# Performance work log

Hardware: AMD Instinct MI355X
Metric: run time of the kernel (lower is better)

Reference implementation:

```python
import jax, jax.numpy as jnp
import numpy as np

B, H, W = 64, 84, 84
IN_F, HID, NCLS = 128, 256, 50
C2 = IN_F * 2  # 256
EPS = 1e-5
K_NEIGH = 4


def _ring_edges(batch):
    rows = np.repeat(np.arange(batch), K_NEIGH)
    offs = np.tile(np.arange(1, K_NEIGH + 1), batch)
    cols = (rows + offs) % batch
    return jnp.asarray(np.stack([rows, cols]), dtype=jnp.int32)


def setup_inputs() -> dict:
    key = jax.random.key(0)
    ks = jax.random.split(key, 40)
    i = iter(range(40))
    def n(shape, s=0.05):
        return jax.random.normal(ks[next(i)], shape, jnp.float32) * s
    def u(shape):
        return jax.random.uniform(ks[next(i)], shape, jnp.float32, 0.5, 1.5)
    d = {}
    d['x'] = jax.random.normal(ks[next(i)], (B, 3, H, W), jnp.float32)
    # conv1 + bn1
    d['conv1_w'] = n((IN_F, 3, 3, 3)); d['conv1_b'] = n((IN_F,))
    d['bn1_g'] = 1.0 + n((IN_F,)); d['bn1_b'] = n((IN_F,))
    d['bn1_m'] = n((IN_F,)); d['bn1_v'] = u((IN_F,))
    # conv2 + bn2
    d['conv2_w'] = n((C2, IN_F, 3, 3)); d['conv2_b'] = n((C2,))
    d['bn2_g'] = 1.0 + n((C2,)); d['bn2_b'] = n((C2,))
    d['bn2_m'] = n((C2,)); d['bn2_v'] = u((C2,))
    # conv3 + bn3
    d['conv3_w'] = n((C2, C2, 3, 3)); d['conv3_b'] = n((C2,))
    d['bn3_g'] = 1.0 + n((C2,)); d['bn3_b'] = n((C2,))
    d['bn3_m'] = n((C2,)); d['bn3_v'] = u((C2,))
    # gcn1: Linear(256,256), attn Linear(512,1)
    d['gcn1_lw'] = n((HID, C2)); d['gcn1_lb'] = n((HID,))
    d['gcn1_aw'] = n((1, 2 * C2)); d['gcn1_ab'] = n((1,))
    # gcn2: Linear(256,256), attn Linear(512,1)
    d['gcn2_lw'] = n((HID, HID)); d['gcn2_lb'] = n((HID,))
    d['gcn2_aw'] = n((1, 2 * HID)); d['gcn2_ab'] = n((1,))
    # fc
    d['fc_w'] = n((NCLS, HID)); d['fc_b'] = n((NCLS,))
    d['edge_index'] = _ring_edges(B)  # [2, 4*B] deterministic ring graph
    return d


def _conv_bn_relu(x, w, b, g, be, m, v):
    y = jax.lax.conv_general_dilated(
        x, w, window_strides=(1, 1), padding='SAME',
        dimension_numbers=('NCHW', 'OIHW', 'NCHW')) + b[None, :, None, None]
    scale = (g / jnp.sqrt(v + EPS))[None, :, None, None]
    y = (y - m[None, :, None, None]) * scale + be[None, :, None, None]
    return jax.nn.relu(y)


def _gcn_conv(h, row, col, lw, lb, aw, ab):
    # h: [N, F]; edge gather -> attn MLP -> global softmax -> scatter-add
    ef = jnp.concatenate([h[row], h[col]], axis=1)          # [E, 2F]
    ew = jax.nn.leaky_relu(ef @ aw.T + ab, 0.01)            # [E, 1]
    ew = jax.nn.softmax(ew, axis=0)                          # softmax over all edges
    agg = jnp.zeros_like(h).at[row].add(h[col] * ew)        # [N, F]
    return agg @ lw.T + lb + h                               # linear + residual


def reference(x, conv1_w, conv1_b, bn1_g, bn1_b, bn1_m, bn1_v,
              conv2_w, conv2_b, bn2_g, bn2_b, bn2_m, bn2_v,
              conv3_w, conv3_b, bn3_g, bn3_b, bn3_m, bn3_v,
              gcn1_lw, gcn1_lb, gcn1_aw, gcn1_ab,
              gcn2_lw, gcn2_lb, gcn2_aw, gcn2_ab,
              fc_w, fc_b, edge_index):
    h = _conv_bn_relu(x, conv1_w, conv1_b, bn1_g, bn1_b, bn1_m, bn1_v)
    h = _conv_bn_relu(h, conv2_w, conv2_b, bn2_g, bn2_b, bn2_m, bn2_v)
    h = _conv_bn_relu(h, conv3_w, conv3_b, bn3_g, bn3_b, bn3_m, bn3_v)
    h = h.mean(axis=(2, 3))                                  # adaptive avg pool 1x1 + flatten -> [B, 256]
    row, col = edge_index[0], edge_index[1]
    h = jax.nn.relu(_gcn_conv(h, row, col, gcn1_lw, gcn1_lb, gcn1_aw, gcn1_ab))
    h = jax.nn.relu(_gcn_conv(h, row, col, gcn2_lw, gcn2_lb, gcn2_aw, gcn2_ab))
    return h @ fc_w.T + fc_b                                 # [B, 50]
```

## Files before the change

kernel.cpp:

```cpp
#include <hip/hip_runtime.h>
#include <hip/hip_bf16.h>

typedef __attribute__((ext_vector_type(8))) short bf16x8;
typedef __attribute__((ext_vector_type(4))) float f32x4;

#define DEV __device__ __forceinline__

static constexpr int Bn   = 64;
static constexpr int Hs   = 84;
static constexpr int HP   = 86;
static constexpr int C1c  = 128;
static constexpr int C2c  = 256;
static constexpr int NPOS = Hs * Hs;
static constexpr float EPSf = 1e-5f;

DEV __hip_bfloat16 f2b(float v) { return __float2bfloat16(v); }

DEV void gload16(const void* g, void* l) {
    __builtin_amdgcn_global_load_lds(
        (const __attribute__((address_space(1))) void*)g,
        (__attribute__((address_space(3))) void*)l, 16, 0, 0);
}

__global__ __launch_bounds__(128) void conv1_k(
    const float* __restrict__ x,
    const float* __restrict__ w,  const float* __restrict__ cb,
    const float* __restrict__ g,  const float* __restrict__ be,
    const float* __restrict__ mm, const float* __restrict__ vv,
    __hip_bfloat16* __restrict__ h1)
{
    __shared__ float xin[3][3][HP];
    int bi = blockIdx.x;
    int b = bi / Hs, y = bi % Hs;
    int t = threadIdx.x;

    for (int idx = t; idx < 3 * 3 * HP; idx += 128) {
        int ci = idx / (3 * HP);
        int r  = idx % (3 * HP);
        int dy = r / HP;
        int xx = r % HP;
        int iy = y + dy - 1;
        int ix = xx - 1;
        float v = 0.f;
        if (iy >= 0 && iy < Hs && ix >= 0 && ix < Hs)
            v = x[((size_t)(b * 3 + ci) * Hs + iy) * Hs + ix];
        xin[ci][dy][xx] = v;
    }
    int co = t;
    float wr[3][3][3];
    for (int ci = 0; ci < 3; ci++)
        for (int dy = 0; dy < 3; dy++)
            for (int dx = 0; dx < 3; dx++)
                wr[ci][dy][dx] = w[((co * 3 + ci) * 3 + dy) * 3 + dx];
    float scale = g[co] / sqrtf(vv[co] + EPSf);
    float bias  = (cb[co] - mm[co]) * scale + be[co];
    __syncthreads();

    for (int xp = 0; xp < Hs; xp++) {
        float acc = 0.f;
        #pragma unroll
        for (int ci = 0; ci < 3; ci++)
            #pragma unroll
            for (int dy = 0; dy < 3; dy++)
                #pragma unroll
                for (int dx = 0; dx < 3; dx++)
                    acc += xin[ci][dy][xp + dx] * wr[ci][dy][dx];
        float o = acc * scale + bias;
        o = o > 0.f ? o : 0.f;
        h1[((size_t)(b * HP + y + 1) * HP + (xp + 1)) * C1c + co] = f2b(o);
    }
}

template <int C>
__global__ void halo_zero(__hip_bfloat16* __restrict__ h)
{
    int i = blockIdx.x;
    int b = i / 340, p = i % 340;
    int y, xx;
    if (p < 86)       { y = 0;  xx = p; }
    else if (p < 172) { y = 85; xx = p - 86; }
    else if (p < 256) { xx = 0; y = p - 172 + 1; }
    else              { xx = 85; y = p - 256 + 1; }
    h[((size_t)(b * HP + y) * HP + xx) * C + threadIdx.x] = f2b(0.f);
}

template <int CIN>
__global__ void prep_w(const float* __restrict__ w, __hip_bfloat16* __restrict__ wm)
{
    int e  = blockIdx.x * 256 + threadIdx.x;
    int k  = e >> 8;
    int co = e & 255;
    int tap = k / CIN;
    int ci  = k % CIN;
    int ty = tap / 3, tx = tap % 3;
    wm[(size_t)(k >> 5) * 8192 + co * 32 + (k & 31)] =
        f2b(w[((size_t)(co * CIN + ci) * 3 + ty) * 3 + tx]);
}

__global__ void prep_sb(const float* __restrict__ cb, const float* __restrict__ g,
                        const float* __restrict__ be, const float* __restrict__ mm,
                        const float* __restrict__ vv, float* __restrict__ sb)
{
    int co = threadIdx.x;
    float s = g[co] / sqrtf(vv[co] + EPSf);
    sb[co] = s;
    sb[256 + co] = (cb[co] - mm[co]) * s + be[co];
}

__global__ void zero_f32(float* __restrict__ p)
{
    p[blockIdx.x * 256 + threadIdx.x] = 0.f;
}

template <int CIN, bool POOL>
__global__ __launch_bounds__(512, 2) void conv_igemm(
    const __hip_bfloat16* __restrict__ in, const __hip_bfloat16* __restrict__ wgt,
    const float* __restrict__ sb, __hip_bfloat16* __restrict__ out, float* __restrict__ pool)
{
    constexpr int KB = CIN / 32;
    constexpr int NK = 9 * KB / 2;
    constexpr unsigned BUF = 49152u;
    __shared__ __align__(16) char lds[3 * 49152];
    __shared__ float pl[512];

    int t = threadIdx.x;
    int l = t & 63, w = t >> 6;
    int lidx = l & 15, lg = l >> 4;
    int wm = w >> 2, wn = w & 3;

    int nwg  = (int)gridDim.x;
    int orig = (int)blockIdx.x;
    int xcd = orig & 7, idx = orig >> 3;
    int q = nwg >> 3, r = nwg & 7;
    int bx = (xcd < r ? xcd * (q + 1) : r * (q + 1) + (xcd - r) * q) + idx;
    int m0 = bx * 128;

    int seg  = (t & 3) ^ ((t >> 3) & 3);
    int srow = t >> 2;
    const __hip_bfloat16* pA;
    {
        int gm = m0 + srow;
        int b0 = gm / NPOS; int r0 = gm - b0 * NPOS;
        int y0 = r0 / Hs;   int x0 = r0 - y0 * Hs;
        pA = in + ((size_t)(b0 * HP + y0) * HP + x0) * CIN + seg * 8;
    }
    const __hip_bfloat16* pB = wgt + (size_t)srow * 32 + seg * 8;

    int swz = (lidx >> 1) & 3;
    unsigned aRd[4][2], bRd[4][2];
    #pragma unroll
    for (int mf = 0; mf < 4; mf++)
        #pragma unroll
        for (int kh = 0; kh < 2; kh++)
            aRd[mf][kh] = (unsigned)(kh * 8192 + (wm * 64 + mf * 16 + lidx) * 64 + ((lg ^ swz) * 16));
    #pragma unroll
    for (int nf = 0; nf < 4; nf++)
        #pragma unroll
        for (int kh = 0; kh < 2; kh++)
            bRd[nf][kh] = (unsigned)(16384 + kh * 16384 + (wn * 64 + nf * 16 + lidx) * 64 + ((lg ^ swz) * 16));

    f32x4 acc[4][4];
    #pragma unroll
    for (int i = 0; i < 4; i++)
        #pragma unroll
        for (int j = 0; j < 4; j++)
            acc[i][j] = (f32x4){0.f, 0.f, 0.f, 0.f};
    if (POOL) pl[t] = 0.f;

    auto AOFF = [&](int s) -> size_t {
        int kb = s / 9, tap = s - kb * 9;
        int ty = tap / 3, tx = tap - ty * 3;
        return (size_t)(ty * HP + tx) * CIN + kb * 32;
    };
    auto BOFF = [&](int s) -> size_t {
        int kb = s / 9, tap = s - kb * 9;
        return (size_t)(tap * KB + kb) * 8192;
    };
    auto ISSUE_P0 = [&](int kt2, unsigned nb) {
        int s0 = 2 * kt2, s1 = s0 + 1;
        gload16(pA + AOFF(s0), lds + nb +          w * 1024);
        gload16(pA + AOFF(s1), lds + nb +  8192 + w * 1024);
        gload16(pB + BOFF(s0), lds + nb + 16384 + w * 1024);
    };
    auto ISSUE_P1 = [&](int kt2, unsigned nb) {
        int s0 = 2 * kt2, s1 = s0 + 1;
        gload16(pB + BOFF(s0) + 4096, lds + nb + 24576 + w * 1024);
        gload16(pB + BOFF(s1),        lds + nb + 32768 + w * 1024);
        gload16(pB + BOFF(s1) + 4096, lds + nb + 40960 + w * 1024);
    };

    ISSUE_P0(0, 0u); ISSUE_P1(0, 0u);
    ISSUE_P0(1, BUF); ISSUE_P1(1, BUF);

    for (int kt = 0; kt < NK; ++kt) {
        unsigned cb = (unsigned)(kt % 3) * BUF;
        unsigned nb = (unsigned)((kt + 2) % 3) * BUF;
        bool more = (kt + 2) < NK;

        if (kt + 1 < NK) asm volatile("s_waitcnt vmcnt(6)" ::: "memory");
        else             asm volatile("s_waitcnt vmcnt(0)" ::: "memory");
        __builtin_amdgcn_s_barrier();

        bf16x8 av[4][2], bv0[2][2];
        #pragma unroll
        for (int mf = 0; mf < 4; mf++)
            #pragma unroll
            for (int kh = 0; kh < 2; kh++)
                av[mf][kh] = *(const bf16x8*)(lds + cb + aRd[mf][kh]);
        #pragma unroll
        for (int nf = 0; nf < 2; nf++)
            #pragma unroll
            for (int kh = 0; kh < 2; kh++)
                bv0[nf][kh] = *(const bf16x8*)(lds + cb + bRd[nf][kh]);
        if (more) ISSUE_P0(kt + 2, nb);
        __builtin_amdgcn_s_barrier();
        asm volatile("s_waitcnt lgkmcnt(0)" ::: "memory");
        __builtin_amdgcn_sched_barrier(0);
        __builtin_amdgcn_s_setprio(1);
        #pragma unroll
        for (int kh = 0; kh < 2; kh++)
            #pragma unroll
            for (int mf = 0; mf < 4; mf++)
                #pragma unroll
                for (int nf = 0; nf < 2; nf++)
                    acc[mf][nf] = __builtin_amdgcn_mfma_f32_16x16x32_bf16(
                        av[mf][kh], bv0[nf][kh], acc[mf][nf], 0, 0, 0);
        __builtin_amdgcn_s_setprio(0);

        __builtin_amdgcn_s_barrier();
        bf16x8 bv1[2][2];
        #pragma unroll
        for (int nf = 0; nf < 2; nf++)
            #pragma unroll
            for (int kh = 0; kh < 2; kh++)
                bv1[nf][kh] = *(const bf16x8*)(lds + cb + bRd[2 + nf][kh]);
        if (more) ISSUE_P1(kt + 2, nb);
        __builtin_amdgcn_s_barrier();
        asm volatile("s_waitcnt lgkmcnt(0)" ::: "memory");
        __builtin_amdgcn_sched_barrier(0);
        __builtin_amdgcn_s_setprio(1);
        #pragma unroll
        for (int kh = 0; kh < 2; kh++)
            #pragma unroll
            for (int mf = 0; mf < 4; mf++)
                #pragma unroll
                for (int nf = 0; nf < 2; nf++)
                    acc[mf][2 + nf] = __builtin_amdgcn_mfma_f32_16x16x32_bf16(
                        av[mf][kh], bv1[nf][kh], acc[mf][2 + nf], 0, 0, 0);
        __builtin_amdgcn_s_setprio(0);
    }

    float sc[4], bi2[4];
    #pragma unroll
    for (int nf = 0; nf < 4; nf++) {
        int cn = wn * 64 + nf * 16 + lidx;
        sc[nf]  = sb[cn];
        bi2[nf] = sb[256 + cn];
    }

    if (!POOL) {
        #pragma unroll
        for (int mf = 0; mf < 4; mf++) {
            #pragma unroll
            for (int r2 = 0; r2 < 4; r2++) {
                int row = wm * 64 + mf * 16 + lg * 4 + r2;
                int gm2 = m0 + row;
                int b2  = gm2 / NPOS;
                int rm2 = gm2 - b2 * NPOS;
                int y2  = rm2 / Hs;
                int x2  = rm2 - y2 * Hs;
                size_t ob = ((size_t)(b2 * HP + y2 + 1) * HP + (x2 + 1)) * 256;
                #pragma unroll
                for (int nf = 0; nf < 4; nf++) {
                    float v = acc[mf][nf][r2] * sc[nf] + bi2[nf];
                    v = v > 0.f ? v : 0.f;
                    out[ob + wn * 64 + nf * 16 + lidx] = f2b(v);
                }
            }
        }
    } else {
        int bs_lo   = m0 / NPOS;
        int row_lim = (bs_lo + 1) * NPOS - m0;
        __builtin_amdgcn_s_barrier();
        #pragma unroll
        for (int nf = 0; nf < 4; nf++) {
            float s0 = 0.f, s1 = 0.f;
            #pragma unroll
            for (int mf = 0; mf < 4; mf++)
                #pragma unroll
                for (int r2 = 0; r2 < 4; r2++) {
                    int row = wm * 64 + mf * 16 + lg * 4 + r2;
                    float v = acc[mf][nf][r2] * sc[nf] + bi2[nf];
                    v = v > 0.f ? v : 0.f;
                    if (row < row_lim) s0 += v; else s1 += v;
                }
            int cl = wn * 64 + nf * 16 + lidx;
            atomicAdd(&pl[cl], s0);
            if (row_lim < 128) atomicAdd(&pl[256 + cl], s1);
        }
        __syncthreads();
        if (t < 256)
            atomicAdd(&pool[bs_lo * 256 + t], pl[t]);
        else if (row_lim < 128)
            atomicAdd(&pool[(bs_lo + 1) * 256 + (t - 256)], pl[t]);
    }
}

__global__ void pool_div(const float* __restrict__ pool, float* __restrict__ h0)
{
    int i = blockIdx.x * 256 + threadIdx.x;
    h0[i] = pool[i] * (1.0f / (float)NPOS);
}

__global__ __launch_bounds__(256) void gcn_attn(
    const float* __restrict__ h, const float* __restrict__ aw,
    const float* __restrict__ ab, const int* __restrict__ ei,
    float* __restrict__ ew)
{
    __shared__ float p[64], q[64], red[256];
    int t = threadIdx.x;
    if (t < 64) {
        float pp = 0.f, qq = 0.f;
        for (int c = 0; c < 256; c++) {
            float hv = h[t * 256 + c];
            pp += hv * aw[c];
            qq += hv * aw[256 + c];
        }
        p[t] = pp; q[t] = qq;
    }
    __syncthreads();
    int r = ei[t], c = ei[256 + t];
    float s = p[r] + q[c] + ab[0];
    s = s >= 0.f ? s : 0.01f * s;
    red[t] = s;
    __syncthreads();
    for (int st = 128; st > 0; st >>= 1) {
        if (t < st) red[t] = fmaxf(red[t], red[t + st]);
        __syncthreads();
    }
    float mx = red[0];
    __syncthreads();
    float e = expf(s - mx);
    red[t] = e;
    __syncthreads();
    for (int st = 128; st > 0; st >>= 1) {
        if (t < st) red[t] += red[t + st];
        __syncthreads();
    }
    ew[t] = e / red[0];
}

__global__ __launch_bounds__(256) void gcn_agg(
    const float* __restrict__ h, const float* __restrict__ ew, const int* __restrict__ ei,
    const float* __restrict__ lw, const float* __restrict__ lb,
    float* __restrict__ ho)
{
    __shared__ float agg[256];
    __shared__ float ewl[256];
    __shared__ int rl[256], cl[256];
    int n = blockIdx.x;
    int t = threadIdx.x;
    ewl[t] = ew[t];
    rl[t] = ei[t];
    cl[t] = ei[256 + t];
    __syncthreads();
    float a = 0.f;
    for (int e = 0; e < 256; e++)
        if (rl[e] == n) a += ewl[e] * h[cl[e] * 256 + t];
    agg[t] = a;
    __syncthreads();
    float o = 0.f;
    for (int c2 = 0; c2 < 256; c2++)
        o += agg[c2] * lw[t * 256 + c2];
    o += lb[t] + h[n * 256 + t];
    o = o > 0.f ? o : 0.f;
    ho[n * 256 + t] = o;
}

__global__ void fc_k(const float* __restrict__ h, const float* __restrict__ fw,
                     const float* __restrict__ fb, float* __restrict__ out)
{
    int n = blockIdx.x;
    int t = threadIdx.x;
    if (t < 50) {
        float o = 0.f;
        for (int c = 0; c < 256; c++)
            o += h[n * 256 + c] * fw[t * 256 + c];
        o += fb[t];
        out[n * 50 + t] = o;
    }
}

extern "C" void kernel_launch(void* const* d_in, const int* in_sizes, int n_in,
                              void* d_out, int out_size, void* d_ws, size_t ws_size,
                              hipStream_t stream)
{
    (void)in_sizes; (void)n_in; (void)out_size;

    const float* X    = (const float*)d_in[0];
    const float* c1w  = (const float*)d_in[1];
    const float* c1b  = (const float*)d_in[2];
    const float* b1g  = (const float*)d_in[3];
    const float* b1b  = (const float*)d_in[4];
    const float* b1m  = (const float*)d_in[5];
    const float* b1v  = (const float*)d_in[6];
    const float* c2w  = (const float*)d_in[7];
    const float* c2b  = (const float*)d_in[8];
    const float* b2g  = (const float*)d_in[9];
    const float* b2b  = (const float*)d_in[10];
    const float* b2m  = (const float*)d_in[11];
    const float* b2v  = (const float*)d_in[12];
    const float* c3w  = (const float*)d_in[13];
    const float* c3b  = (const float*)d_in[14];
    const float* b3g  = (const float*)d_in[15];
    const float* b3b  = (const float*)d_in[16];
    const float* b3m  = (const float*)d_in[17];
    const float* b3v  = (const float*)d_in[18];
    const float* g1lw = (const float*)d_in[19];
    const float* g1lb = (const float*)d_in[20];
    const float* g1aw = (const float*)d_in[21];
    const float* g1ab = (const float*)d_in[22];
    const float* g2lw = (const float*)d_in[23];
    const float* g2lb = (const float*)d_in[24];
    const float* g2aw = (const float*)d_in[25];
    const float* g2ab = (const float*)d_in[26];
    const float* fcw  = (const float*)d_in[27];
    const float* fcb  = (const float*)d_in[28];
    const int*   EI   = (const int*)d_in[29];

    size_t fixedB = 3000000;
    int chb = 8;
    if (ws_size >= (size_t)64 * 5680128 + fixedB)      chb = 64;
    else if (ws_size >= (size_t)32 * 5680128 + fixedB) chb = 32;
    else if (ws_size >= (size_t)16 * 5680128 + fixedB) chb = 16;
    int nchunks = Bn / chb;
    int mch = chb * NPOS;

    char* p = (char*)d_ws;
    auto carve = [&](size_t bytes) {
        char* r = p;
        p += (bytes + 255) & ~(size_t)255;
        return r;
    };
    __hip_bfloat16* h1c = (__hip_bfloat16*)carve((size_t)chb * HP * HP * C1c * 2);
    __hip_bfloat16* h2c = (__hip_bfloat16*)carve((size_t)chb * HP * HP * C2c * 2);
    __hip_bfloat16* wm2 = (__hip_bfloat16*)carve((size_t)9 * C1c * 256 * 2);
    __hip_bfloat16* wm3 = (__hip_bfloat16*)carve((size_t)9 * C2c * 256 * 2);
    float* sb2  = (float*)carve(512 * 4);
    float* sb3  = (float*)carve(512 * 4);
    float* pool = (float*)carve(64 * 256 * 4);
    float* h0   = (float*)carve(64 * 256 * 4);
    float* hg1  = (float*)carve(64 * 256 * 4);
    float* hg2  = (float*)carve(64 * 256 * 4);
    float* ew1  = (float*)carve(256 * 4);
    float* ew2  = (float*)carve(256 * 4);

    halo_zero<C1c><<<dim3(chb * 340), dim3(C1c), 0, stream>>>(h1c);
    halo_zero<C2c><<<dim3(chb * 340), dim3(C2c), 0, stream>>>(h2c);
    prep_w<C1c><<<dim3(9 * C1c), dim3(256), 0, stream>>>(c2w, wm2);
    prep_w<C2c><<<dim3(9 * C2c), dim3(256), 0, stream>>>(c3w, wm3);
    prep_sb<<<dim3(1), dim3(256), 0, stream>>>(c2b, b2g, b2b, b2m, b2v, sb2);
    prep_sb<<<dim3(1), dim3(256), 0, stream>>>(c3b, b3g, b3b, b3m, b3v, sb3);
    zero_f32<<<dim3(64), dim3(256), 0, stream>>>(pool);

    for (int ch = 0; ch < nchunks; ch++) {
        const float* xch = X + (size_t)ch * chb * 3 * NPOS;
        conv1_k<<<dim3(chb * Hs), dim3(C1c), 0, stream>>>(
            xch, c1w, c1b, b1g, b1b, b1m, b1v, h1c);
        conv_igemm<C1c, false><<<dim3(mch / 128), dim3(512), 0, stream>>>(
            h1c, wm2, sb2, h2c, nullptr);
        conv_igemm<C2c, true ><<<dim3(mch / 128), dim3(512), 0, stream>>>(
            h2c, wm3, sb3, nullptr, pool + (size_t)ch * chb * 256);
    }
    pool_div<<<dim3(64), dim3(256), 0, stream>>>(pool, h0);

    gcn_attn<<<dim3(1), dim3(256), 0, stream>>>(h0, g1aw, g1ab, EI, ew1);
    gcn_agg<<<dim3(64), dim3(256), 0, stream>>>(h0, ew1, EI, g1lw, g1lb, hg1);
    gcn_attn<<<dim3(1), dim3(256), 0, stream>>>(hg1, g2aw, g2ab, EI, ew2);
    gcn_agg<<<dim3(64), dim3(256), 0, stream>>>(hg1, ew2, EI, g2lw, g2lb, hg2);
    fc_k<<<dim3(64), dim3(64), 0, stream>>>(hg2, fcw, fcb, (float*)d_out);
}
```

Measured before the change: 1.014 ms.

## Enlarge conv implicit-GEMM M tile to 256 with double-buffered LDS pipeline

Doubles the per-block output tile from 128 to 256 rows so each wave computes 8x4 MFMA fragments, reusing each loaded B fragment across twice as many A rows. The LDS pipeline changes from triple-buffered 48KB stages to double-buffered 64KB stages, and loads are issued per k-half with a one-stage prefetch. Grid size halves and the pooling epilogue limits are updated. The larger accumulator array raises register pressure against the (512,2) launch bounds, the 128KB of LDS may cut occupancy, and the shallower prefetch could expose memory latency. The minimum chunk size also rises from 8 to 16 batches.

```diff
diff --git a/kernel.cpp b/kernel.cpp
--- a/kernel.cpp
+++ b/kernel.cpp
@@ -119,8 +119,8 @@
 {
     constexpr int KB = CIN / 32;
     constexpr int NK = 9 * KB / 2;
-    constexpr unsigned BUF = 49152u;
-    __shared__ __align__(16) char lds[3 * 49152];
+    constexpr unsigned BUFSZ = 65536u;
+    __shared__ __align__(16) char lds[2 * 65536];
     __shared__ float pl[512];
 
     int t = threadIdx.x;
@@ -133,35 +133,40 @@
     int xcd = orig & 7, idx = orig >> 3;
     int q = nwg >> 3, r = nwg & 7;
     int bx = (xcd < r ? xcd * (q + 1) : r * (q + 1) + (xcd - r) * q) + idx;
-    int m0 = bx * 128;
+    int m0 = bx * 256;
 
     int seg  = (t & 3) ^ ((t >> 3) & 3);
     int srow = t >> 2;
-    const __hip_bfloat16* pA;
+    const __hip_bfloat16 *pA0, *pA1;
     {
         int gm = m0 + srow;
         int b0 = gm / NPOS; int r0 = gm - b0 * NPOS;
         int y0 = r0 / Hs;   int x0 = r0 - y0 * Hs;
-        pA = in + ((size_t)(b0 * HP + y0) * HP + x0) * CIN + seg * 8;
-    }
-    const __hip_bfloat16* pB = wgt + (size_t)srow * 32 + seg * 8;
+        pA0 = in + ((size_t)(b0 * HP + y0) * HP + x0) * CIN + seg * 8;
+        gm = m0 + 128 + srow;
+        b0 = gm / NPOS; r0 = gm - b0 * NPOS;
+        y0 = r0 / Hs;   x0 = r0 - y0 * Hs;
+        pA1 = in + ((size_t)(b0 * HP + y0) * HP + x0) * CIN + seg * 8;
+    }
+    const __hip_bfloat16* pB0 = wgt + (size_t)srow * 32 + seg * 8;
+    const __hip_bfloat16* pB1 = wgt + (size_t)(128 + srow) * 32 + seg * 8;
 
     int swz = (lidx >> 1) & 3;
-    unsigned aRd[4][2], bRd[4][2];
+    unsigned aRd[8][2], bRd[4][2];
     #pragma unroll
-    for (int mf = 0; mf < 4; mf++)
+    for (int mf = 0; mf < 8; mf++)
         #pragma unroll
         for (int kh = 0; kh < 2; kh++)
-            aRd[mf][kh] = (unsigned)(kh * 8192 + (wm * 64 + mf * 16 + lidx) * 64 + ((lg ^ swz) * 16));
+            aRd[mf][kh] = (unsigned)(kh * 16384 + (wm * 128 + mf * 16 + lidx) * 64 + ((lg ^ swz) * 16));
     #pragma unroll
     for (int nf = 0; nf < 4; nf++)
         #pragma unroll
         for (int kh = 0; kh < 2; kh++)
-            bRd[nf][kh] = (unsigned)(16384 + kh * 16384 + (wn * 64 + nf * 16 + lidx) * 64 + ((lg ^ swz) * 16));
-
-    f32x4 acc[4][4];
+            bRd[nf][kh] = (unsigned)(32768 + kh * 16384 + (wn * 64 + nf * 16 + lidx) * 64 + ((lg ^ swz) * 16));
+
+    f32x4 acc[8][4];
     #pragma unroll
-    for (int i = 0; i < 4; i++)
+    for (int i = 0; i < 8; i++)
         #pragma unroll
         for (int j = 0; j < 4; j++)
             acc[i][j] = (f32x4){0.f, 0.f, 0.f, 0.f};
@@ -176,78 +181,68 @@
         int kb = s / 9, tap = s - kb * 9;
         return (size_t)(tap * KB + kb) * 8192;
     };
-    auto ISSUE_P0 = [&](int kt2, unsigned nb) {
-        int s0 = 2 * kt2, s1 = s0 + 1;
-        gload16(pA + AOFF(s0), lds + nb +          w * 1024);
-        gload16(pA + AOFF(s1), lds + nb +  8192 + w * 1024);
-        gload16(pB + BOFF(s0), lds + nb + 16384 + w * 1024);
+    auto ISSUE = [&](int kt2, int kh, unsigned bb) {
+        int s = 2 * kt2 + kh;
+        size_t ao = AOFF(s), bo = BOFF(s);
+        unsigned ap = bb + (unsigned)(kh * 16384) + (unsigned)(w * 1024);
+        unsigned bp = bb + 32768u + (unsigned)(kh * 16384) + (unsigned)(w * 1024);
+        gload16(pA0 + ao, lds + ap);
+        gload16(pA1 + ao, lds + ap + 8192);
+        gload16(pB0 + bo, lds + bp);
+        gload16(pB1 + bo, lds + bp + 8192);
     };
-    auto ISSUE_P1 = [&](int kt2, unsigned nb) {
-        int s0 = 2 * kt2, s1 = s0 + 1;
-        gload16(pB + BOFF(s0) + 4096, lds + nb + 24576 + w * 1024);
-        gload16(pB + BOFF(s1),        lds + nb + 32768 + w * 1024);
-        gload16(pB + BOFF(s1) + 4096, lds + nb + 40960 + w * 1024);
-    };
-
-    ISSUE_P0(0, 0u); ISSUE_P1(0, 0u);
-    ISSUE_P0(1, BUF); ISSUE_P1(1, BUF);
+
+    ISSUE(0, 0, 0u);
+    ISSUE(0, 1, 0u);
 
     for (int kt = 0; kt < NK; ++kt) {
-        unsigned cb = (unsigned)(kt % 3) * BUF;
-        unsigned nb = (unsigned)((kt + 2) % 3) * BUF;
-        bool more = (kt + 2) < NK;
-
-        if (kt + 1 < NK) asm volatile("s_waitcnt vmcnt(6)" ::: "memory");
-        else             asm volatile("s_waitcnt vmcnt(0)" ::: "memory");
-        __builtin_amdgcn_s_barrier();
-
-        bf16x8 av[4][2], bv0[2][2];
-        #pragma unroll
-        for (int mf = 0; mf < 4; mf++)
-            #pragma unroll
-            for (int kh = 0; kh < 2; kh++)
-                av[mf][kh] = *(const bf16x8*)(lds + cb + aRd[mf][kh]);
-        #pragma unroll
-        for (int nf = 0; nf < 2; nf++)
-            #pragma unroll
-            for (int kh = 0; kh < 2; kh++)
-                bv0[nf][kh] = *(const bf16x8*)(lds + cb + bRd[nf][kh]);
-        if (more) ISSUE_P0(kt + 2, nb);
-        __builtin_amdgcn_s_barrier();
-        asm volatile("s_waitcnt lgkmcnt(0)" ::: "memory");
-        __builtin_amdgcn_sched_barrier(0);
-        __builtin_amdgcn_s_setprio(1);
-        #pragma unroll
-        for (int kh = 0; kh < 2; kh++)
+        unsigned cb = (kt & 1) ? BUFSZ : 0u;
+        unsigned nb = (kt & 1) ? 0u : BUFSZ;
+        bool more = (kt + 1) < NK;
+
+        #pragma unroll
+        for (int kh = 0; kh < 2; ++kh) {
+            if (kh == 0 || more) asm volatile("s_waitcnt vmcnt(4)" ::: "memory");
+            else                 asm volatile("s_waitcnt vmcnt(0)" ::: "memory");
+            __builtin_amdgcn_s_barrier();
+
+            bf16x8 av[4], bv[4];
+            #pragma unroll
+            for (int mf = 0; mf < 4; mf++)
+                av[mf] = *(const bf16x8*)(lds + cb + aRd[mf][kh]);
+            #pragma unroll
+            for (int nf = 0; nf < 4; nf++)
+                bv[nf] = *(const bf16x8*)(lds + cb + bRd[nf][kh]);
+            if (more) ISSUE(kt + 1, kh, nb);
+            __builtin_amdgcn_s_barrier();
+            asm volatile("s_waitcnt lgkmcnt(0)" ::: "memory");
+            __builtin_amdgcn_sched_barrier(0);
+            __builtin_amdgcn_s_setprio(1);
             #pragma unroll
             for (int mf = 0; mf < 4; mf++)
                 #pragma unroll
-                for (int nf = 0; nf < 2; nf++)
+                for (int nf = 0; nf < 4; nf++)
                     acc[mf][nf] = __builtin_amdgcn_mfma_f32_16x16x32_bf16(
-                        av[mf][kh], bv0[nf][kh], acc[mf][nf], 0, 0, 0);
-        __builtin_amdgcn_s_setprio(0);
-
-        __builtin_amdgcn_s_barrier();
-        bf16x8 bv1[2][2];
-        #pragma unroll
-        for (int nf = 0; nf < 2; nf++)
-            #pragma unroll
-            for (int kh = 0; kh < 2; kh++)
-                bv1[nf][kh] = *(const bf16x8*)(lds + cb + bRd[2 + nf][kh]);
-        if (more) ISSUE_P1(kt + 2, nb);
-        __builtin_amdgcn_s_barrier();
-        asm volatile("s_waitcnt lgkmcnt(0)" ::: "memory");
-        __builtin_amdgcn_sched_barrier(0);
-        __builtin_amdgcn_s_setprio(1);
-        #pragma unroll
-        for (int kh = 0; kh < 2; kh++)
+                        av[mf], bv[nf], acc[mf][nf], 0, 0, 0);
+            __builtin_amdgcn_s_setprio(0);
+
+            __builtin_amdgcn_s_barrier();
+            bf16x8 av2[4];
+            #pragma unroll
+            for (int mf = 0; mf < 4; mf++)
+                av2[mf] = *(const bf16x8*)(lds + cb + aRd[4 + mf][kh]);
+            __builtin_amdgcn_s_barrier();
+            asm volatile("s_waitcnt lgkmcnt(0)" ::: "memory");
+            __builtin_amdgcn_sched_barrier(0);
+            __builtin_amdgcn_s_setprio(1);
             #pragma unroll
             for (int mf = 0; mf < 4; mf++)
                 #pragma unroll
-                for (int nf = 0; nf < 2; nf++)
-                    acc[mf][2 + nf] = __builtin_amdgcn_mfma_f32_16x16x32_bf16(
-                        av[mf][kh], bv1[nf][kh], acc[mf][2 + nf], 0, 0, 0);
-        __builtin_amdgcn_s_setprio(0);
+                for (int nf = 0; nf < 4; nf++)
+                    acc[4 + mf][nf] = __builtin_amdgcn_mfma_f32_16x16x32_bf16(
+                        av2[mf], bv[nf], acc[4 + mf][nf], 0, 0, 0);
+            __builtin_amdgcn_s_setprio(0);
+        }
     }
 
     float sc[4], bi2[4];
@@ -260,10 +255,10 @@
 
     if (!POOL) {
         #pragma unroll
-        for (int mf = 0; mf < 4; mf++) {
+        for (int mf = 0; mf < 8; mf++) {
             #pragma unroll
             for (int r2 = 0; r2 < 4; r2++) {
-                int row = wm * 64 + mf * 16 + lg * 4 + r2;
+                int row = wm * 128 + mf * 16 + lg * 4 + r2;
                 int gm2 = m0 + row;
                 int b2  = gm2 / NPOS;
                 int rm2 = gm2 - b2 * NPOS;
@@ -286,22 +281,22 @@
         for (int nf = 0; nf < 4; nf++) {
             float s0 = 0.f, s1 = 0.f;
             #pragma unroll
-            for (int mf = 0; mf < 4; mf++)
+            for (int mf = 0; mf < 8; mf++)
                 #pragma unroll
                 for (int r2 = 0; r2 < 4; r2++) {
-                    int row = wm * 64 + mf * 16 + lg * 4 + r2;
+                    int row = wm * 128 + mf * 16 + lg * 4 + r2;
                     float v = acc[mf][nf][r2] * sc[nf] + bi2[nf];
                     v = v > 0.f ? v : 0.f;
                     if (row < row_lim) s0 += v; else s1 += v;
                 }
             int cl = wn * 64 + nf * 16 + lidx;
             atomicAdd(&pl[cl], s0);
-            if (row_lim < 128) atomicAdd(&pl[256 + cl], s1);
+            if (row_lim < 256) atomicAdd(&pl[256 + cl], s1);
         }
         __syncthreads();
         if (t < 256)
             atomicAdd(&pool[bs_lo * 256 + t], pl[t]);
-        else if (row_lim < 128)
+        else if (row_lim < 256)
             atomicAdd(&pool[(bs_lo + 1) * 256 + (t - 256)], pl[t]);
     }
 }
@@ -429,10 +424,9 @@
     const int*   EI   = (const int*)d_in[29];
 
     size_t fixedB = 3000000;
-    int chb = 8;
+    int chb = 16;
     if (ws_size >= (size_t)64 * 5680128 + fixedB)      chb = 64;
     else if (ws_size >= (size_t)32 * 5680128 + fixedB) chb = 32;
-    else if (ws_size >= (size_t)16 * 5680128 + fixedB) chb = 16;
     int nchunks = Bn / chb;
     int mch = chb * NPOS;
 
@@ -467,9 +461,9 @@
         const float* xch = X + (size_t)ch * chb * 3 * NPOS;
         conv1_k<<<dim3(chb * Hs), dim3(C1c), 0, stream>>>(
             xch, c1w, c1b, b1g, b1b, b1m, b1v, h1c);
-        conv_igemm<C1c, false><<<dim3(mch / 128), dim3(512), 0, stream>>>(
+        conv_igemm<C1c, false><<<dim3(mch / 256), dim3(512), 0, stream>>>(
             h1c, wm2, sb2, h2c, nullptr);
-        conv_igemm<C2c, true ><<<dim3(mch / 128), dim3(512), 0, stream>>>(
+        conv_igemm<C2c, true ><<<dim3(mch / 256), dim3(512), 0, stream>>>(
             h2c, wm3, sb3, nullptr, pool + (size_t)ch * chb * 256);
     }
     pool_div<<<dim3(64), dim3(256), 0, stream>>>(pool, h0);
```

Result: no change. 1.007 ms (-0.7%).
